# Optimization experiments

Hardware: AMD Instinct MI355X
Metric: run time of the kernel (lower is better)

The kernel has to match this reference:

```python
import jax, jax.numpy as jnp
import numpy as np

A_COEF, B_COEF, C_COEF = 1.0, 0.1, 10.0
KL_COEF = 0.005
EPS = 1e-6

B, P1, F, P2 = 32, 778, 1538, 3000
PARAM_DIM, LATENT = 61, 64


def setup_inputs() -> dict:
    key = jax.random.key(0)
    ks = jax.random.split(key, 9)
    return {
        "recon_x": jax.random.normal(ks[0], (B, PARAM_DIM), jnp.float32),
        "x": jax.random.normal(ks[1], (B, PARAM_DIM), jnp.float32),
        "mu": jax.random.normal(ks[2], (B, LATENT), jnp.float32),
        "logvar": jax.random.normal(ks[3], (B, LATENT), jnp.float32),
        "recon_xyz": jax.random.normal(ks[4], (B, P1, 3), jnp.float32),
        "hand_xyz": jax.random.normal(ks[5], (B, P1, 3), jnp.float32),
        "hand_faces": jax.random.randint(ks[6], (B, F, 3), 0, P1, jnp.int64),
        "obj_pts": jax.random.normal(ks[7], (B, P2, 3), jnp.float32),
        "v_weights": jax.random.uniform(ks[8], (P1,), jnp.float32),
    }


def _verts_normals_single(verts, faces):
    # verts: (V,3), faces: (F,3). PyTorch3D-style area-weighted vertex normals.
    v0 = verts[faces[:, 0]]
    v1 = verts[faces[:, 1]]
    v2 = verts[faces[:, 2]]
    fn = jnp.cross(v1 - v0, v2 - v0)  # (F,3) ~ 2*area*face_normal
    n = (jnp.zeros_like(verts)
         .at[faces[:, 0]].add(fn)
         .at[faces[:, 1]].add(fn)
         .at[faces[:, 2]].add(fn))
    norm = jnp.linalg.norm(n, axis=-1, keepdims=True)
    return n / jnp.maximum(norm, EPS)


_verts_normals = jax.vmap(_verts_normals_single)


def _sqdist(xp, yp):
    # (B,P1,P2) pairwise squared distances
    x2 = jnp.sum(xp * xp, axis=-1)[:, :, None]
    y2 = jnp.sum(yp * yp, axis=-1)[:, None, :]
    return x2 + y2 - 2.0 * jnp.einsum('bpd,bqd->bpq', xp, yp)


def _point2point_signed(xp, yp, x_normals):
    # xp: (B,P1,3) hand, yp: (B,P2,3) object, x_normals: (B,P1,3)
    d2 = _sqdist(xp, yp)
    xidx = jnp.argmin(d2, axis=2)  # (B,P1) nearest object point per hand vert
    yidx = jnp.argmin(d2, axis=1)  # (B,P2) nearest hand vert per object point
    x_near = jnp.take_along_axis(yp, xidx[..., None], axis=1)  # (B,P1,3)
    y_near = jnp.take_along_axis(xp, yidx[..., None], axis=1)  # (B,P2,3)
    x2y = xp - x_near
    y2x = yp - y_near
    y_nn = jnp.take_along_axis(x_normals, yidx[..., None], axis=1)  # (B,P2,3)
    in_out = jnp.sign(jnp.sum(y_nn * y2x, axis=-1))
    y2x_signed = jnp.linalg.norm(y2x, axis=2) * in_out  # (B,P2)
    x2y_signed = jnp.linalg.norm(x2y, axis=2)           # (B,P1)
    return y2x_signed, x2y_signed


def _loss_cnet(verts_rhand, verts_rhand_gt, faces, verts_obj, v_weights):
    v_w2 = jnp.power(v_weights, 1.0 / 2.5)
    rh_n = _verts_normals(verts_rhand, faces)
    rh_n_gt = _verts_normals(verts_rhand_gt, faces)
    o2h, h2o = _point2point_signed(verts_rhand, verts_obj, rh_n)
    o2h_gt, h2o_gt = _point2point_signed(verts_rhand_gt, verts_obj, rh_n_gt)
    w_dist = (o2h_gt < 0.01) & (o2h_gt > -0.005)
    w_neg = o2h < 0.0
    w = jnp.where(w_neg, 1.5, jnp.where(w_dist, 1.0, 0.1))
    loss_h = 35.0 * (1.0 - KL_COEF) * jnp.mean(jnp.abs(jnp.abs(h2o) - jnp.abs(h2o_gt)) * v_w2)
    loss_o = 30.0 * (1.0 - KL_COEF) * jnp.mean(jnp.abs(o2h - o2h_gt) * w)
    return loss_h + loss_o


def reference(recon_x, x, mu, logvar, recon_xyz, hand_xyz, hand_faces, obj_pts, v_weights):
    bsz = recon_x.shape[0]
    param_loss = jnp.sum((recon_x - x) ** 2) / bsz
    recon_loss = jnp.sum((recon_xyz - hand_xyz) ** 2) / hand_xyz.shape[0]
    KLD = -0.5 * jnp.sum(1.0 + logvar - mu ** 2 - jnp.exp(logvar)) / hand_xyz.shape[0]
    cvae_loss = recon_loss + KLD
    ho_loss = _loss_cnet(recon_xyz, hand_xyz, hand_faces, obj_pts, v_weights)
    loss = A_COEF * cvae_loss + B_COEF * param_loss + C_COEF * ho_loss
    return loss, param_loss, ho_loss, recon_loss, KLD
```

## Files before the change

kernel.cpp:

```cpp
#include <hip/hip_runtime.h>
#include <math.h>

#define B 32
#define P1 778
#define NF 1538
#define P2 3000
#define PARAM_DIM 61
#define LATENT 64

#define NCH_O2H 4
#define CH_O2H 768
#define NCH_H2O 15
#define CH_H2O 200
#define RED1_BLKS 16
#define HC_BLKS 128
#define OC_BLKS 192
#define HALF_F 769

#define D1_NRM 128
#define D1_TOT (D1_NRM + RED1_BLKS)
#define D2_O2H (NCH_O2H * 64)
#define D2_H2O (NCH_H2O * 64)
#define D2_TOT (D2_O2H + D2_H2O)
#define D3_TOT (OC_BLKS + HC_BLKS)

#define NP_OFF  0
#define NP_SZ   (2*2*B*P1*4)
#define OS_OFF  (NP_OFF + NP_SZ)
#define OS_SZ   (2*B*P2)
#define HP_OFF  (OS_OFF + OS_SZ)
#define HP_SZ   (NCH_H2O*2*B*P1)
#define R1_OFF  (HP_OFF + HP_SZ)
#define RH_OFF  (R1_OFF + RED1_BLKS*3)
#define RO_OFF  (RH_OFF + HC_BLKS)

__global__ __launch_bounds__(256) void kd1(
    const float* __restrict__ recon_x, const float* __restrict__ x,
    const float* __restrict__ mu, const float* __restrict__ logvar,
    const float* __restrict__ recon_xyz, const float* __restrict__ hand_xyz,
    const int* __restrict__ faces, float* __restrict__ ws) {
  __shared__ float4 sv[P1];
  __shared__ float sn[4][2336];
  const int tid = threadIdx.x;
  const int bid = blockIdx.x;

  if (bid < D1_NRM) {
    const int half = bid >> 6, r = bid & 63, set = r >> 5, b = r & 31;
    const float* verts = (set == 0 ? recon_xyz : hand_xyz) + b * P1 * 3;
    const int* f = faces + b * NF * 3 + half * HALF_F * 3;
    const int nf = (half == 0) ? HALF_F : (NF - HALF_F);
    for (int i = tid; i < P1; i += 256)
      sv[i] = make_float4(verts[3*i], verts[3*i+1], verts[3*i+2], 0.f);
    for (int i = tid; i < 4 * 2336; i += 256) ((float*)sn)[i] = 0.f;
    __syncthreads();
    float* s = sn[tid >> 6];
    for (int k = tid; k < nf; k += 256) {
      int i0 = f[3*k], i1 = f[3*k+1], i2 = f[3*k+2];
      float4 v0 = sv[i0], v1 = sv[i1], v2 = sv[i2];
      float e0x = v1.x - v0.x, e0y = v1.y - v0.y, e0z = v1.z - v0.z;
      float e1x = v2.x - v0.x, e1y = v2.y - v0.y, e1z = v2.z - v0.z;
      float fx = e0y * e1z - e0z * e1y;
      float fy = e0z * e1x - e0x * e1z;
      float fz = e0x * e1y - e0y * e1x;
      atomicAdd(&s[3*i0+0], fx); atomicAdd(&s[3*i0+1], fy); atomicAdd(&s[3*i0+2], fz);
      atomicAdd(&s[3*i1+0], fx); atomicAdd(&s[3*i1+1], fy); atomicAdd(&s[3*i1+2], fz);
      atomicAdd(&s[3*i2+0], fx); atomicAdd(&s[3*i2+1], fy); atomicAdd(&s[3*i2+2], fz);
    }
    __syncthreads();
    float4* np = (float4*)(ws + NP_OFF) + (size_t)((half * 2 + set) * B + b) * P1;
    for (int p = tid; p < P1; p += 256) {
      float nx = sn[0][3*p] + sn[1][3*p] + sn[2][3*p] + sn[3][3*p];
      float ny = sn[0][3*p+1] + sn[1][3*p+1] + sn[2][3*p+1] + sn[3][3*p+1];
      float nz = sn[0][3*p+2] + sn[1][3*p+2] + sn[2][3*p+2] + sn[3][3*p+2];
      np[p] = make_float4(nx, ny, nz, 0.f);
    }
  } else {
    const int blk = bid - D1_NRM;
    const int gtid = blk * 256 + tid, stride = RED1_BLKS * 256;
    float sp = 0.f, sr = 0.f, sk = 0.f;
    for (int i = gtid; i < B * PARAM_DIM; i += stride) { float d = recon_x[i] - x[i]; sp += d * d; }
    for (int i = gtid; i < B * P1 * 3; i += stride)    { float d = recon_xyz[i] - hand_xyz[i]; sr += d * d; }
    for (int i = gtid; i < B * LATENT; i += stride)    { float lv = logvar[i], m = mu[i]; sk += 1.f + lv - m * m - expf(lv); }
    for (int off = 32; off > 0; off >>= 1) {
      sp += __shfl_down(sp, off, 64);
      sr += __shfl_down(sr, off, 64);
      sk += __shfl_down(sk, off, 64);
    }
    float* sred = (float*)sn;
    const int wv = tid >> 6;
    if ((tid & 63) == 0) { sred[wv*3] = sp; sred[wv*3+1] = sr; sred[wv*3+2] = sk; }
    __syncthreads();
    if (tid == 0) {
      float a = 0.f, bb = 0.f, c = 0.f;
      for (int w = 0; w < 4; ++w) { a += sred[w*3]; bb += sred[w*3+1]; c += sred[w*3+2]; }
      ws[R1_OFF + blk*3+0] = a; ws[R1_OFF + blk*3+1] = bb; ws[R1_OFF + blk*3+2] = c;
    }
  }
}

__global__ __launch_bounds__(256) void kd2(
    const float* __restrict__ recon_xyz, const float* __restrict__ hand_xyz,
    const float* __restrict__ obj, float* __restrict__ ws) {
  __shared__ float4 s4[P1];
  const int tid = threadIdx.x;
  const int bid = blockIdx.x;

  if (bid < D2_O2H) {
    const int chunk = bid >> 6, r = bid & 63, set = r >> 5, b = r & 31;
    const float* verts = (set == 0 ? recon_xyz : hand_xyz) + b * P1 * 3;
    for (int i = tid; i < P1; i += 256) {
      float vx = verts[3*i], vy = verts[3*i+1], vz = verts[3*i+2];
      s4[i] = make_float4(vx, vy, vz, vx*vx + vy*vy + vz*vz + 64.f);
    }
    __syncthreads();
    const int q0 = chunk * CH_O2H + tid;
    const int q1 = q0 + 256;
    const int q2 = q0 + 512;
    const bool act2 = q2 < P2;
    const float* op = obj + (size_t)b * P2 * 3;
    float p0x = op[3*q0], p0y = op[3*q0+1], p0z = op[3*q0+2];
    float p1x = op[3*q1], p1y = op[3*q1+1], p1z = op[3*q1+2];
    float p2x = 0.f, p2y = 0.f, p2z = 0.f;
    if (act2) { p2x = op[3*q2]; p2y = op[3*q2+1]; p2z = op[3*q2+2]; }
    const float a0 = -2.f*p0x, b0 = -2.f*p0y, c0 = -2.f*p0z;
    const float a1 = -2.f*p1x, b1 = -2.f*p1y, c1 = -2.f*p1z;
    const float a2 = -2.f*p2x, b2 = -2.f*p2y, c2 = -2.f*p2z;
    unsigned best0 = 0xFFFFFFFFu, best1 = 0xFFFFFFFFu, best2 = 0xFFFFFFFFu;
    #pragma unroll 4
    for (int p = 0; p < P1; p += 2) {
      float4 h0 = s4[p], h1 = s4[p+1];
      float d00 = fmaf(h0.x, a0, fmaf(h0.y, b0, fmaf(h0.z, c0, h0.w)));
      float d01 = fmaf(h1.x, a0, fmaf(h1.y, b0, fmaf(h1.z, c0, h1.w)));
      float d10 = fmaf(h0.x, a1, fmaf(h0.y, b1, fmaf(h0.z, c1, h0.w)));
      float d11 = fmaf(h1.x, a1, fmaf(h1.y, b1, fmaf(h1.z, c1, h1.w)));
      float d20 = fmaf(h0.x, a2, fmaf(h0.y, b2, fmaf(h0.z, c2, h0.w)));
      float d21 = fmaf(h1.x, a2, fmaf(h1.y, b2, fmaf(h1.z, c2, h1.w)));
      unsigned k00 = (__float_as_uint(d00) & 0xFFFFFC00u) | (unsigned)p;
      unsigned k01 = (__float_as_uint(d01) & 0xFFFFFC00u) | (unsigned)(p+1);
      unsigned k10 = (__float_as_uint(d10) & 0xFFFFFC00u) | (unsigned)p;
      unsigned k11 = (__float_as_uint(d11) & 0xFFFFFC00u) | (unsigned)(p+1);
      unsigned k20 = (__float_as_uint(d20) & 0xFFFFFC00u) | (unsigned)p;
      unsigned k21 = (__float_as_uint(d21) & 0xFFFFFC00u) | (unsigned)(p+1);
      unsigned n0 = k00 < k01 ? k00 : k01;
      unsigned n1 = k10 < k11 ? k10 : k11;
      unsigned n2 = k20 < k21 ? k20 : k21;
      best0 = n0 < best0 ? n0 : best0;
      best1 = n1 < best1 ? n1 : best1;
      best2 = n2 < best2 ? n2 : best2;
    }
    const float4* np0 = (const float4*)(ws + NP_OFF) + (size_t)(set * B + b) * P1;
    const float4* np1 = np0 + (size_t)2 * B * P1;
    float* os = ws + OS_OFF + (size_t)(set * B + b) * P2;
    {
      int bi = (int)(best0 & 1023u); bi = bi < P1 ? bi : P1 - 1;
      float4 h = s4[bi]; float4 na = np0[bi], nb = np1[bi];
      float nx = na.x + nb.x, ny = na.y + nb.y, nz = na.z + nb.z;
      float dx = p0x - h.x, dy = p0y - h.y, dz = p0z - h.z;
      float d2 = fmaf(dx, dx, fmaf(dy, dy, dz * dz));
      float dt = nx * dx + ny * dy + nz * dz;
      float sg = (dt > 0.f) ? 1.f : ((dt < 0.f) ? -1.f : 0.f);
      os[q0] = sqrtf(d2) * sg;
    }
    {
      int bi = (int)(best1 & 1023u); bi = bi < P1 ? bi : P1 - 1;
      float4 h = s4[bi]; float4 na = np0[bi], nb = np1[bi];
      float nx = na.x + nb.x, ny = na.y + nb.y, nz = na.z + nb.z;
      float dx = p1x - h.x, dy = p1y - h.y, dz = p1z - h.z;
      float d2 = fmaf(dx, dx, fmaf(dy, dy, dz * dz));
      float dt = nx * dx + ny * dy + nz * dz;
      float sg = (dt > 0.f) ? 1.f : ((dt < 0.f) ? -1.f : 0.f);
      os[q1] = sqrtf(d2) * sg;
    }
    if (act2) {
      int bi = (int)(best2 & 1023u); bi = bi < P1 ? bi : P1 - 1;
      float4 h = s4[bi]; float4 na = np0[bi], nb = np1[bi];
      float nx = na.x + nb.x, ny = na.y + nb.y, nz = na.z + nb.z;
      float dx = p2x - h.x, dy = p2y - h.y, dz = p2z - h.z;
      float d2 = fmaf(dx, dx, fmaf(dy, dy, dz * dz));
      float dt = nx * dx + ny * dy + nz * dz;
      float sg = (dt > 0.f) ? 1.f : ((dt < 0.f) ? -1.f : 0.f);
      os[q2] = sqrtf(d2) * sg;
    }

  } else {
    const int t = bid - D2_O2H;
    const int chunk = t >> 6, r = t & 63, set = r >> 5, b = r & 31;
    const float* verts = (set == 0 ? recon_xyz : hand_xyz) + b * P1 * 3;
    const float* op = obj + (size_t)(b * P2 + chunk * CH_H2O) * 3;
    for (int i = tid; i < CH_H2O; i += 256) {
      float ox = op[3*i], oy = op[3*i+1], oz = op[3*i+2];
      s4[i] = make_float4(ox, oy, oz, ox*ox + oy*oy + oz*oz);
    }
    __syncthreads();
    float* part = ws + HP_OFF + (size_t)((chunk * 2 + set) * B + b) * P1;
    const int p0 = tid, p1 = tid + 256, p2 = tid + 512;
    float ax = verts[3*p0], ay = verts[3*p0+1], az = verts[3*p0+2];
    float bx = verts[3*p1], by = verts[3*p1+1], bz = verts[3*p1+2];
    float cx = verts[3*p2], cy = verts[3*p2+1], cz = verts[3*p2+2];
    float h2a = ax*ax+ay*ay+az*az, h2b = bx*bx+by*by+bz*bz, h2c = cx*cx+cy*cy+cz*cz;
    float nax = -2.f*ax, nay = -2.f*ay, naz = -2.f*az;
    float nbx = -2.f*bx, nby = -2.f*by, nbz = -2.f*bz;
    float ncx = -2.f*cx, ncy = -2.f*cy, ncz = -2.f*cz;
    float m0 = 3.0e38f, m1 = 3.0e38f, m2 = 3.0e38f;
    #pragma unroll 4
    for (int qq = 0; qq < CH_H2O; ++qq) {
      float4 o = s4[qq];
      m0 = fminf(m0, fmaf(o.x, nax, fmaf(o.y, nay, fmaf(o.z, naz, o.w))));
      m1 = fminf(m1, fmaf(o.x, nbx, fmaf(o.y, nby, fmaf(o.z, nbz, o.w))));
      m2 = fminf(m2, fmaf(o.x, ncx, fmaf(o.y, ncy, fmaf(o.z, ncz, o.w))));
    }
    part[p0] = m0 + h2a;
    part[p1] = m1 + h2b;
    part[p2] = m2 + h2c;
    if (tid < P1 - 768) {
      const int p3 = 768 + tid;
      float tx = verts[3*p3], ty = verts[3*p3+1], tz = verts[3*p3+2];
      float h2t = tx*tx+ty*ty+tz*tz;
      float ntx = -2.f*tx, nty = -2.f*ty, ntz = -2.f*tz;
      float m3 = 3.0e38f;
      for (int qq = 0; qq < CH_H2O; ++qq) {
        float4 o = s4[qq];
        m3 = fminf(m3, fmaf(o.x, ntx, fmaf(o.y, nty, fmaf(o.z, ntz, o.w))));
      }
      part[p3] = m3 + h2t;
    }
  }
}

__global__ __launch_bounds__(256) void kd3(const float* __restrict__ vw,
                                           float* __restrict__ ws) {
  __shared__ float sred[4];
  const int tid = threadIdx.x;
  const int bid = blockIdx.x;
  if (bid < OC_BLKS) {
    const int gtid = bid * 256 + tid, stride = OC_BLKS * 256;
    float so = 0.f;
    for (int i = gtid; i < B * P2; i += stride) {
      float osA = ws[OS_OFF + i];
      float osB = ws[OS_OFF + (size_t)B * P2 + i];
      bool wdist = (osB < 0.01f) && (osB > -0.005f);
      float w = (osA < 0.f) ? 1.5f : (wdist ? 1.f : 0.1f);
      so += fabsf(osA - osB) * w;
    }
    for (int off = 32; off > 0; off >>= 1) so += __shfl_down(so, off, 64);
    if ((tid & 63) == 0) sred[tid >> 6] = so;
    __syncthreads();
    if (tid == 0) ws[RO_OFF + bid] = sred[0] + sred[1] + sred[2] + sred[3];
  } else {
    const int blk = bid - OC_BLKS;
    const int gtid = blk * 256 + tid, stride = HC_BLKS * 256;
    float sh = 0.f;
    for (int i = gtid; i < B * P1; i += stride) {
      const int p = i % P1;
      float m0 = 3.0e38f, m1 = 3.0e38f;
      #pragma unroll
      for (int c = 0; c < NCH_H2O; ++c) {
        m0 = fminf(m0, ws[HP_OFF + (size_t)(c*2+0) * B * P1 + i]);
        m1 = fminf(m1, ws[HP_OFF + (size_t)(c*2+1) * B * P1 + i]);
      }
      m0 = fmaxf(m0, 0.f); m1 = fmaxf(m1, 0.f);
      sh += fabsf(sqrtf(m0) - sqrtf(m1)) * powf(vw[p], 0.4f);
    }
    for (int off = 32; off > 0; off >>= 1) sh += __shfl_down(sh, off, 64);
    if ((tid & 63) == 0) sred[tid >> 6] = sh;
    __syncthreads();
    if (tid == 0) ws[RH_OFF + blk] = sred[0] + sred[1] + sred[2] + sred[3];
  }
}

__global__ void kfin(const float* __restrict__ ws, float* __restrict__ out) {
  const int lane = threadIdx.x;
  float sp = 0.f, sr = 0.f, sk = 0.f, sh = 0.f, so = 0.f;
  for (int i = lane; i < RED1_BLKS; i += 64) {
    sp += ws[R1_OFF + i*3+0]; sr += ws[R1_OFF + i*3+1]; sk += ws[R1_OFF + i*3+2];
  }
  for (int i = lane; i < HC_BLKS; i += 64) sh += ws[RH_OFF + i];
  for (int i = lane; i < OC_BLKS; i += 64) so += ws[RO_OFF + i];
  for (int off = 32; off > 0; off >>= 1) {
    sp += __shfl_down(sp, off, 64);
    sr += __shfl_down(sr, off, 64);
    sk += __shfl_down(sk, off, 64);
    sh += __shfl_down(sh, off, 64);
    so += __shfl_down(so, off, 64);
  }
  if (lane == 0) {
    float param_loss = sp / (float)B;
    float recon_loss = sr / (float)B;
    float KLD = -0.5f * sk / (float)B;
    float cvae = recon_loss + KLD;
    float loss_h = 35.f * (1.f - 0.005f) * sh / (float)(B * P1);
    float loss_o = 30.f * (1.f - 0.005f) * so / (float)(B * P2);
    float ho = loss_h + loss_o;
    out[0] = cvae + 0.1f * param_loss + 10.f * ho;
    out[1] = param_loss;
    out[2] = ho;
    out[3] = recon_loss;
    out[4] = KLD;
  }
}

extern "C" void kernel_launch(void* const* d_in, const int* in_sizes, int n_in,
                              void* d_out, int out_size, void* d_ws, size_t ws_size,
                              hipStream_t stream) {
  const float* recon_x   = (const float*)d_in[0];
  const float* x         = (const float*)d_in[1];
  const float* mu        = (const float*)d_in[2];
  const float* logvar    = (const float*)d_in[3];
  const float* recon_xyz = (const float*)d_in[4];
  const float* hand_xyz  = (const float*)d_in[5];
  const int*   faces     = (const int*)d_in[6];
  const float* obj       = (const float*)d_in[7];
  const float* vw        = (const float*)d_in[8];
  float* ws = (float*)d_ws;
  float* out = (float*)d_out;

  kd1<<<dim3(D1_TOT), 256, 0, stream>>>(recon_x, x, mu, logvar,
                                        recon_xyz, hand_xyz, faces, ws);
  kd2<<<dim3(D2_TOT), 256, 0, stream>>>(recon_xyz, hand_xyz, obj, ws);
  kd3<<<dim3(D3_TOT), 256, 0, stream>>>(vw, ws);
  kfin<<<1, 64, 0, stream>>>(ws, out);
}
```

Measured before the change: 127.0 us.

## Compute pairwise distances with bf16 MFMA using split hi/lo precision

```diff
diff --git a/kernel.cpp b/kernel.cpp
--- a/kernel.cpp
+++ b/kernel.cpp
@@ -8,10 +8,12 @@
 #define PARAM_DIM 61
 #define LATENT 64
 
-#define NCH_O2H 4
-#define CH_O2H 768
-#define NCH_H2O 15
-#define CH_H2O 200
+#define P1PAD 784
+#define NTH 49
+#define CHO 768
+#define NTO 12
+#define NPART 16
+
 #define RED1_BLKS 16
 #define HC_BLKS 128
 #define OC_BLKS 192
@@ -19,9 +21,7 @@
 
 #define D1_NRM 128
 #define D1_TOT (D1_NRM + RED1_BLKS)
-#define D2_O2H (NCH_O2H * 64)
-#define D2_H2O (NCH_H2O * 64)
-#define D2_TOT (D2_O2H + D2_H2O)
+#define D2_TOT 256
 #define D3_TOT (OC_BLKS + HC_BLKS)
 
 #define NP_OFF  0
@@ -29,10 +29,18 @@
 #define OS_OFF  (NP_OFF + NP_SZ)
 #define OS_SZ   (2*B*P2)
 #define HP_OFF  (OS_OFF + OS_SZ)
-#define HP_SZ   (NCH_H2O*2*B*P1)
+#define HP_SZ   (NPART*2*B*P1PAD)
 #define R1_OFF  (HP_OFF + HP_SZ)
 #define RH_OFF  (R1_OFF + RED1_BLKS*3)
 #define RO_OFF  (RH_OFF + HC_BLKS)
+
+typedef __attribute__((ext_vector_type(8))) short bf16x8;
+typedef __attribute__((ext_vector_type(4))) float f32x4;
+union U4 { uint4 u; bf16x8 v; };
+
+static __device__ __forceinline__ unsigned umin2(unsigned a, unsigned b) { return a < b ? a : b; }
+static __device__ __forceinline__ unsigned bhi(float x) { return __float_as_uint(x) >> 16; }
+static __device__ __forceinline__ float bres(float x, unsigned h) { return x - __uint_as_float(h << 16); }
 
 __global__ __launch_bounds__(256) void kd1(
     const float* __restrict__ recon_x, const float* __restrict__ x,
@@ -98,131 +106,156 @@
   }
 }
 
-__global__ __launch_bounds__(256) void kd2(
+__global__ __launch_bounds__(256, 1) void kd2(
     const float* __restrict__ recon_xyz, const float* __restrict__ hand_xyz,
     const float* __restrict__ obj, float* __restrict__ ws) {
-  __shared__ float4 s4[P1];
+  __shared__ float4 sVerts[P1PAD];
+  __shared__ float4 sObj[CHO];
+  __shared__ uint4  sPack4[(NTH + 1) * 32];
+  __shared__ unsigned sKeys[CHO];
+  __shared__ uint4  sZero;
+
   const int tid = threadIdx.x;
   const int bid = blockIdx.x;
-
-  if (bid < D2_O2H) {
-    const int chunk = bid >> 6, r = bid & 63, set = r >> 5, b = r & 31;
-    const float* verts = (set == 0 ? recon_xyz : hand_xyz) + b * P1 * 3;
-    for (int i = tid; i < P1; i += 256) {
-      float vx = verts[3*i], vy = verts[3*i+1], vz = verts[3*i+2];
-      s4[i] = make_float4(vx, vy, vz, vx*vx + vy*vy + vz*vz + 64.f);
-    }
-    __syncthreads();
-    const int q0 = chunk * CH_O2H + tid;
-    const int q1 = q0 + 256;
-    const int q2 = q0 + 512;
-    const bool act2 = q2 < P2;
-    const float* op = obj + (size_t)b * P2 * 3;
-    float p0x = op[3*q0], p0y = op[3*q0+1], p0z = op[3*q0+2];
-    float p1x = op[3*q1], p1y = op[3*q1+1], p1z = op[3*q1+2];
-    float p2x = 0.f, p2y = 0.f, p2z = 0.f;
-    if (act2) { p2x = op[3*q2]; p2y = op[3*q2+1]; p2z = op[3*q2+2]; }
-    const float a0 = -2.f*p0x, b0 = -2.f*p0y, c0 = -2.f*p0z;
-    const float a1 = -2.f*p1x, b1 = -2.f*p1y, c1 = -2.f*p1z;
-    const float a2 = -2.f*p2x, b2 = -2.f*p2y, c2 = -2.f*p2z;
-    unsigned best0 = 0xFFFFFFFFu, best1 = 0xFFFFFFFFu, best2 = 0xFFFFFFFFu;
-    #pragma unroll 4
-    for (int p = 0; p < P1; p += 2) {
-      float4 h0 = s4[p], h1 = s4[p+1];
-      float d00 = fmaf(h0.x, a0, fmaf(h0.y, b0, fmaf(h0.z, c0, h0.w)));
-      float d01 = fmaf(h1.x, a0, fmaf(h1.y, b0, fmaf(h1.z, c0, h1.w)));
-      float d10 = fmaf(h0.x, a1, fmaf(h0.y, b1, fmaf(h0.z, c1, h0.w)));
-      float d11 = fmaf(h1.x, a1, fmaf(h1.y, b1, fmaf(h1.z, c1, h1.w)));
-      float d20 = fmaf(h0.x, a2, fmaf(h0.y, b2, fmaf(h0.z, c2, h0.w)));
-      float d21 = fmaf(h1.x, a2, fmaf(h1.y, b2, fmaf(h1.z, c2, h1.w)));
-      unsigned k00 = (__float_as_uint(d00) & 0xFFFFFC00u) | (unsigned)p;
-      unsigned k01 = (__float_as_uint(d01) & 0xFFFFFC00u) | (unsigned)(p+1);
-      unsigned k10 = (__float_as_uint(d10) & 0xFFFFFC00u) | (unsigned)p;
-      unsigned k11 = (__float_as_uint(d11) & 0xFFFFFC00u) | (unsigned)(p+1);
-      unsigned k20 = (__float_as_uint(d20) & 0xFFFFFC00u) | (unsigned)p;
-      unsigned k21 = (__float_as_uint(d21) & 0xFFFFFC00u) | (unsigned)(p+1);
-      unsigned n0 = k00 < k01 ? k00 : k01;
-      unsigned n1 = k10 < k11 ? k10 : k11;
-      unsigned n2 = k20 < k21 ? k20 : k21;
-      best0 = n0 < best0 ? n0 : best0;
-      best1 = n1 < best1 ? n1 : best1;
-      best2 = n2 < best2 ? n2 : best2;
-    }
-    const float4* np0 = (const float4*)(ws + NP_OFF) + (size_t)(set * B + b) * P1;
-    const float4* np1 = np0 + (size_t)2 * B * P1;
-    float* os = ws + OS_OFF + (size_t)(set * B + b) * P2;
-    {
-      int bi = (int)(best0 & 1023u); bi = bi < P1 ? bi : P1 - 1;
-      float4 h = s4[bi]; float4 na = np0[bi], nb = np1[bi];
-      float nx = na.x + nb.x, ny = na.y + nb.y, nz = na.z + nb.z;
-      float dx = p0x - h.x, dy = p0y - h.y, dz = p0z - h.z;
-      float d2 = fmaf(dx, dx, fmaf(dy, dy, dz * dz));
-      float dt = nx * dx + ny * dy + nz * dz;
-      float sg = (dt > 0.f) ? 1.f : ((dt < 0.f) ? -1.f : 0.f);
-      os[q0] = sqrtf(d2) * sg;
-    }
-    {
-      int bi = (int)(best1 & 1023u); bi = bi < P1 ? bi : P1 - 1;
-      float4 h = s4[bi]; float4 na = np0[bi], nb = np1[bi];
-      float nx = na.x + nb.x, ny = na.y + nb.y, nz = na.z + nb.z;
-      float dx = p1x - h.x, dy = p1y - h.y, dz = p1z - h.z;
-      float d2 = fmaf(dx, dx, fmaf(dy, dy, dz * dz));
-      float dt = nx * dx + ny * dy + nz * dz;
-      float sg = (dt > 0.f) ? 1.f : ((dt < 0.f) ? -1.f : 0.f);
-      os[q1] = sqrtf(d2) * sg;
-    }
-    if (act2) {
-      int bi = (int)(best2 & 1023u); bi = bi < P1 ? bi : P1 - 1;
-      float4 h = s4[bi]; float4 na = np0[bi], nb = np1[bi];
-      float nx = na.x + nb.x, ny = na.y + nb.y, nz = na.z + nb.z;
-      float dx = p2x - h.x, dy = p2y - h.y, dz = p2z - h.z;
-      float d2 = fmaf(dx, dx, fmaf(dy, dy, dz * dz));
-      float dt = nx * dx + ny * dy + nz * dz;
-      float sg = (dt > 0.f) ? 1.f : ((dt < 0.f) ? -1.f : 0.f);
-      os[q2] = sqrtf(d2) * sg;
-    }
-
-  } else {
-    const int t = bid - D2_O2H;
-    const int chunk = t >> 6, r = t & 63, set = r >> 5, b = r & 31;
-    const float* verts = (set == 0 ? recon_xyz : hand_xyz) + b * P1 * 3;
-    const float* op = obj + (size_t)(b * P2 + chunk * CH_H2O) * 3;
-    for (int i = tid; i < CH_H2O; i += 256) {
-      float ox = op[3*i], oy = op[3*i+1], oz = op[3*i+2];
-      s4[i] = make_float4(ox, oy, oz, ox*ox + oy*oy + oz*oz);
-    }
-    __syncthreads();
-    float* part = ws + HP_OFF + (size_t)((chunk * 2 + set) * B + b) * P1;
-    const int p0 = tid, p1 = tid + 256, p2 = tid + 512;
-    float ax = verts[3*p0], ay = verts[3*p0+1], az = verts[3*p0+2];
-    float bx = verts[3*p1], by = verts[3*p1+1], bz = verts[3*p1+2];
-    float cx = verts[3*p2], cy = verts[3*p2+1], cz = verts[3*p2+2];
-    float h2a = ax*ax+ay*ay+az*az, h2b = bx*bx+by*by+bz*bz, h2c = cx*cx+cy*cy+cz*cz;
-    float nax = -2.f*ax, nay = -2.f*ay, naz = -2.f*az;
-    float nbx = -2.f*bx, nby = -2.f*by, nbz = -2.f*bz;
-    float ncx = -2.f*cx, ncy = -2.f*cy, ncz = -2.f*cz;
-    float m0 = 3.0e38f, m1 = 3.0e38f, m2 = 3.0e38f;
-    #pragma unroll 4
-    for (int qq = 0; qq < CH_H2O; ++qq) {
-      float4 o = s4[qq];
-      m0 = fminf(m0, fmaf(o.x, nax, fmaf(o.y, nay, fmaf(o.z, naz, o.w))));
-      m1 = fminf(m1, fmaf(o.x, nbx, fmaf(o.y, nby, fmaf(o.z, nbz, o.w))));
-      m2 = fminf(m2, fmaf(o.x, ncx, fmaf(o.y, ncy, fmaf(o.z, ncz, o.w))));
-    }
-    part[p0] = m0 + h2a;
-    part[p1] = m1 + h2b;
-    part[p2] = m2 + h2c;
-    if (tid < P1 - 768) {
-      const int p3 = 768 + tid;
-      float tx = verts[3*p3], ty = verts[3*p3+1], tz = verts[3*p3+2];
-      float h2t = tx*tx+ty*ty+tz*tz;
-      float ntx = -2.f*tx, nty = -2.f*ty, ntz = -2.f*tz;
-      float m3 = 3.0e38f;
-      for (int qq = 0; qq < CH_H2O; ++qq) {
-        float4 o = s4[qq];
-        m3 = fminf(m3, fmaf(o.x, ntx, fmaf(o.y, nty, fmaf(o.z, ntz, o.w))));
-      }
-      part[p3] = m3 + h2t;
+  const int chunk = bid >> 6, rr = bid & 63, set = rr >> 5, b = rr & 31;
+  const float* verts = (set == 0 ? recon_xyz : hand_xyz) + b * P1 * 3;
+  const float* op = obj + (size_t)b * P2 * 3;
+
+  if (tid == 0) sZero = make_uint4(0u, 0u, 0u, 0u);
+  for (int i = tid; i < P1PAD; i += 256) {
+    float vx, vy, vz;
+    if (i < P1) { vx = verts[3*i]; vy = verts[3*i+1]; vz = verts[3*i+2]; }
+    else        { vx = vy = vz = 1.0e6f; }
+    sVerts[i] = make_float4(vx, vy, vz, 0.f);
+  }
+  for (int i = tid; i < CHO; i += 256) {
+    const int q = chunk * CHO + i;
+    float ox, oy, oz;
+    if (q < P2) { ox = op[3*q]; oy = op[3*q+1]; oz = op[3*q+2]; }
+    else        { ox = oy = oz = 1.0e6f; }
+    sObj[i] = make_float4(ox, oy, oz, ox*ox + oy*oy + oz*oz);
+  }
+  __syncthreads();
+
+  for (int idx = tid; idx < NTH * 32; idx += 256) {
+    const int t = idx >> 5, vl = idx & 31, vg = vl >> 4;
+    const float4 v = sVerts[t * 16 + (vl & 15)];
+    const float sx = -2.f * v.x, sy = -2.f * v.y, sz = -2.f * v.z;
+    const unsigned hx = bhi(sx), hy = bhi(sy), hz = bhi(sz);
+    unsigned w0, w1, w2, w3;
+    if (vg == 0) {
+      const unsigned lx = bhi(bres(sx, hx));
+      const unsigned ly = bhi(bres(sy, hy));
+      const unsigned lz = bhi(bres(sz, hz));
+      w0 = hx | (hy << 16);
+      w1 = hz | (lx << 16);
+      w2 = ly | (lz << 16);
+      w3 = hx | (hy << 16);
+    } else {
+      const float h2 = v.x*v.x + v.y*v.y + v.z*v.z;
+      const unsigned h2h = bhi(h2);
+      const unsigned h2l = bhi(bres(h2, h2h));
+      w0 = hz  | (h2h << 16);
+      w1 = h2l | (0x3F80u << 16);
+      w2 = 0x3F80u;
+      w3 = 0u;
+    }
+    sPack4[t * 32 + vl] = make_uint4(w0, w1, w2, w3);
+  }
+
+  const int l = tid & 63, wv = tid >> 6, g = l >> 4, cl = l & 15;
+  U4 bw[NTO];
+  #pragma unroll
+  for (int j = 0; j < NTO; ++j) {
+    const float4 o = sObj[wv * 192 + j * 16 + cl];
+    unsigned u0 = 0u, u1 = 0u, u2 = 0u, u3 = 0u;
+    if (g == 0) {
+      const unsigned ohx = bhi(o.x), ohy = bhi(o.y), ohz = bhi(o.z);
+      const unsigned olx = bhi(bres(o.x, ohx));
+      const unsigned oly = bhi(bres(o.y, ohy));
+      u0 = ohx | (ohy << 16);
+      u1 = ohz | (ohx << 16);
+      u2 = ohy | (ohz << 16);
+      u3 = olx | (oly << 16);
+    } else if (g == 1) {
+      const unsigned ohz = bhi(o.z);
+      const unsigned olz = bhi(bres(o.z, ohz));
+      const float o2p = o.w + 1.0f;
+      const unsigned o2h = bhi(o2p);
+      const unsigned o2l = bhi(bres(o2p, o2h));
+      u0 = olz | (0x3F80u << 16);
+      u1 = 0x3F80u | (o2h << 16);
+      u2 = o2l;
+      u3 = 0u;
+    }
+    bw[j].u = make_uint4(u0, u1, u2, u3);
+  }
+  __syncthreads();
+
+  unsigned om[NTO];
+  #pragma unroll
+  for (int j = 0; j < NTO; ++j) om[j] = 0xFFFFFFFFu;
+
+  float* hpart = ws + HP_OFF + (size_t)(((chunk * 4 + wv) * 2 + set) * B + b) * P1PAD;
+  const f32x4 czero = {0.f, 0.f, 0.f, 0.f};
+
+  const uint4* ap = (l < 32) ? ((const uint4*)sPack4 + l) : &sZero;
+  const int astep = (l < 32) ? 32 : 0;
+  uint4 au = *ap; ap += astep;
+
+  int ib = g * 4;
+  for (int t = 0; t < NTH; ++t, ib += 16) {
+    const uint4 aunx = *ap; ap += astep;
+    U4 ac; ac.u = au;
+    float hm0 = 3.0e38f, hm1 = 3.0e38f, hm2 = 3.0e38f, hm3 = 3.0e38f;
+    #pragma unroll
+    for (int j = 0; j < NTO; ++j) {
+      const f32x4 d = __builtin_amdgcn_mfma_f32_16x16x32_bf16(ac.v, bw[j].v, czero, 0, 0, 0);
+      hm0 = fminf(hm0, d[0]); hm1 = fminf(hm1, d[1]);
+      hm2 = fminf(hm2, d[2]); hm3 = fminf(hm3, d[3]);
+      const unsigned k0 = (__float_as_uint(d[0]) & 0xFFFFFC00u) | (unsigned)(ib + 0);
+      const unsigned k1 = (__float_as_uint(d[1]) & 0xFFFFFC00u) | (unsigned)(ib + 1);
+      const unsigned k2 = (__float_as_uint(d[2]) & 0xFFFFFC00u) | (unsigned)(ib + 2);
+      const unsigned k3 = (__float_as_uint(d[3]) & 0xFFFFFC00u) | (unsigned)(ib + 3);
+      om[j] = umin2(om[j], umin2(umin2(k0, k1), umin2(k2, k3)));
+    }
+    #pragma unroll
+    for (int m = 1; m <= 8; m <<= 1) {
+      hm0 = fminf(hm0, __shfl_xor(hm0, m, 64));
+      hm1 = fminf(hm1, __shfl_xor(hm1, m, 64));
+      hm2 = fminf(hm2, __shfl_xor(hm2, m, 64));
+      hm3 = fminf(hm3, __shfl_xor(hm3, m, 64));
+    }
+    if (cl == 0)
+      *(float4*)&hpart[ib] = make_float4(hm0 - 1.f, hm1 - 1.f, hm2 - 1.f, hm3 - 1.f);
+    au = aunx;
+  }
+
+  #pragma unroll
+  for (int j = 0; j < NTO; ++j) {
+    unsigned v = umin2(om[j], (unsigned)__shfl_xor((int)om[j], 16, 64));
+    v = umin2(v, (unsigned)__shfl_xor((int)v, 32, 64));
+    if (l < 16) sKeys[wv * 192 + j * 16 + l] = v;
+  }
+  __syncthreads();
+
+  const float4* np0 = (const float4*)(ws + NP_OFF) + (size_t)(set * B + b) * P1;
+  const float4* np1 = np0 + (size_t)2 * B * P1;
+  float* os = ws + OS_OFF + (size_t)(set * B + b) * P2;
+  for (int i = tid; i < CHO; i += 256) {
+    const int q = chunk * CHO + i;
+    if (q < P2) {
+      const unsigned key = sKeys[i];
+      int hi = (int)(key & 1023u); if (hi > P1 - 1) hi = P1 - 1;
+      const float4 h = sVerts[hi];
+      const float4 o = sObj[i];
+      const float dx = o.x - h.x, dy = o.y - h.y, dz = o.z - h.z;
+      const float d2 = fmaf(dx, dx, fmaf(dy, dy, dz * dz));
+      const float4 na = np0[hi], nb = np1[hi];
+      const float nx = na.x + nb.x, ny = na.y + nb.y, nz = na.z + nb.z;
+      const float dt = nx * dx + ny * dy + nz * dz;
+      const float sg = (dt > 0.f) ? 1.f : ((dt < 0.f) ? -1.f : 0.f);
+      os[q] = sqrtf(d2) * sg;
     }
   }
 }
@@ -251,12 +284,13 @@
     const int gtid = blk * 256 + tid, stride = HC_BLKS * 256;
     float sh = 0.f;
     for (int i = gtid; i < B * P1; i += stride) {
-      const int p = i % P1;
+      const int p = i % P1, bb = i / P1;
+      const size_t base0 = (size_t)HP_OFF + (size_t)bb * P1PAD + p;
       float m0 = 3.0e38f, m1 = 3.0e38f;
       #pragma unroll
-      for (int c = 0; c < NCH_H2O; ++c) {
-        m0 = fminf(m0, ws[HP_OFF + (size_t)(c*2+0) * B * P1 + i]);
-        m1 = fminf(m1, ws[HP_OFF + (size_t)(c*2+1) * B * P1 + i]);
+      for (int c = 0; c < NPART; ++c) {
+        m0 = fminf(m0, ws[base0 + (size_t)(c*2+0) * B * P1PAD]);
+        m1 = fminf(m1, ws[base0 + (size_t)(c*2+1) * B * P1PAD]);
       }
       m0 = fmaxf(m0, 0.f); m1 = fmaxf(m1, 0.f);
       sh += fabsf(sqrtf(m0) - sqrtf(m1)) * powf(vw[p], 0.4f);
```

Result: slower. 137.6 us (+8.3%).
